# Kernel tuning notes

Measured on AMD Instinct MI355X. Metric: run time of the kernel, lower is better.

## Reference

```python
import jax, jax.numpy as jnp
import numpy as np

N = 50000        # nodes
E = 500000       # edges
NUM = 4          # sampled intermediate neighbors per edge (self.num)
F = 64           # in_feats == out_feats (transform=False)
D = 32           # dist_dim
NB = 64          # embedding rows = len(boundaries)+1


def setup_inputs() -> dict:
    key = jax.random.key(0)
    ks = jax.random.split(key, 10)
    feat = jax.random.normal(ks[0], (N, F), jnp.float32)
    loc = jax.random.uniform(ks[1], (N, 3), jnp.float32)          # 3D positions in unit cube
    boundaries = jnp.sort(jax.random.uniform(ks[2], (NB - 1,), jnp.float32, 0.0, 2.0))
    embed_table = jax.random.normal(ks[3], (NB, D), jnp.float32)
    G_w = jax.random.normal(ks[4], (F, D), jnp.float32) / np.sqrt(D)      # Linear(dist_dim->out, no bias)
    agg_w = jax.random.normal(ks[5], (F, 2 * F), jnp.float32) / np.sqrt(2 * F)  # Linear(2*out->out)
    agg_b = jnp.zeros((F,), jnp.float32)
    src = jax.random.randint(ks[6], (E,), 0, N, jnp.int32)
    dst = jax.random.randint(ks[7], (E,), 0, N, jnp.int32)
    inter_ids = jax.random.randint(ks[8], (E, NUM), 0, N, jnp.int32)
    return dict(feat=feat, loc=loc, boundaries=boundaries, embed_table=embed_table,
                G_w=G_w, agg_w=agg_w, agg_b=agg_b, src=src, dst=dst, inter_ids=inter_ids)


def reference(feat, loc, boundaries, embed_table, G_w, agg_w, agg_b, src, dst, inter_ids):
    n = feat.shape[0]
    ones = jnp.ones((src.shape[0],), feat.dtype)
    # symmetric-ish degree normalization: d0 = in_deg^-0.5, d2 = out_deg^-0.5
    in_deg = jax.ops.segment_sum(ones, dst, num_segments=n)
    out_deg = jax.ops.segment_sum(ones, src, num_segments=n)
    d0 = jnp.clip(in_deg, 1.0) ** -0.5   # [N]
    d2 = jnp.clip(out_deg, 1.0) ** -0.5  # [N]

    # dist1 = ||loc[dst] - loc[src]||_2, bucketize -> embed -> G
    dist1 = jnp.linalg.norm(loc[dst] - loc[src], axis=1)              # [E]
    de1 = embed_table[jnp.searchsorted(boundaries, dist1)] @ G_w.T    # [E, F]

    # intermediate sampled neighbors: dist to each sampled node from edge src
    pos_src = loc[src]                                                # [E, 3]
    inter_pos = loc[inter_ids]                                        # [E, NUM, 3]
    dist_ = jnp.linalg.norm(pos_src[:, None, :] - inter_pos, axis=-1) # [E, NUM]
    de_ = embed_table[jnp.searchsorted(boundaries, dist_)] @ G_w.T    # [E, NUM, F]
    inter_h = feat[inter_ids]                                         # [E, NUM, F]
    dist_embed_dot_h = (de_ * inter_h).mean(axis=1)                   # [E, F]

    # h = d0[dst] * d2[src] * agg_fc([de1 * h_src, dist_embed_dot_h])
    cat = jnp.concatenate([de1 * feat[src], dist_embed_dot_h], axis=1)  # [E, 2F]
    msg = (d0[dst] * d2[src])[:, None] * (cat @ agg_w.T + agg_b)        # [E, F]

    # update_all(copy_e('h'), sum) -> scatter-sum messages to dst
    ft = jax.ops.segment_sum(msg, dst, num_segments=n)                  # [N, F]
    return ft
```

## Files before the change

### kernel.cpp

```cpp
#include <hip/hip_runtime.h>
#include <math.h>

#define LUTN 1024
#define LUTSCALE 512.0f
#define NBINS 50048
#define CHSH 12


__global__ __launch_bounds__(256) void prep_kernel(
    const float* __restrict__ embed, const float* __restrict__ G_w,
    const float* __restrict__ boundaries, const float* __restrict__ feat,
    const float* __restrict__ loc,
    float* __restrict__ M, int* __restrict__ lut,
    unsigned short* __restrict__ featH, float4* __restrict__ loc4, int N) {

    const int gid = blockIdx.x * 256 + threadIdx.x;
    const int gsz = gridDim.x * 256;
    for (int i = gid; i < 4096; i += gsz) {
        int b = i >> 6, f = i & 63;
        float acc = 0.f;
        #pragma unroll
        for (int dd = 0; dd < 32; ++dd) acc += embed[b * 32 + dd] * G_w[f * 32 + dd];
        M[i] = acc;
    }
    for (int i = gid; i < LUTN; i += gsz) {
        float left = (float)i * (1.0f / LUTSCALE);
        int c = 0;
        for (int j = 0; j < 63; ++j) c += (boundaries[j] < left) ? 1 : 0;
        lut[i] = c;
    }
    const int nq = N * 16;
    for (int i = gid; i < nq; i += gsz) {
        float4 v = ((const float4*)feat)[i];
        unsigned ux = __float_as_uint(v.x), uy = __float_as_uint(v.y);
        unsigned uz = __float_as_uint(v.z), uw = __float_as_uint(v.w);
        ushort4 h;
        h.x = (unsigned short)((ux + 0x7FFFu + ((ux >> 16) & 1u)) >> 16);
        h.y = (unsigned short)((uy + 0x7FFFu + ((uy >> 16) & 1u)) >> 16);
        h.z = (unsigned short)((uz + 0x7FFFu + ((uz >> 16) & 1u)) >> 16);
        h.w = (unsigned short)((uw + 0x7FFFu + ((uw >> 16) & 1u)) >> 16);
        ((ushort4*)featH)[i] = h;
    }
    for (int i = gid; i < N; i += gsz)
        loc4[i] = make_float4(loc[3 * i], loc[3 * i + 1], loc[3 * i + 2], 0.f);
}


__global__ __launch_bounds__(512) void hist_kernel(
    const int* __restrict__ src, const int* __restrict__ dst,
    unsigned char* __restrict__ pcnt, unsigned char* __restrict__ psrc,
    unsigned char* __restrict__ rnk8, int E) {

    __shared__ unsigned int h[NBINS / 4];
    for (int i = threadIdx.x; i < NBINS / 4; i += 512) h[i] = 0u;
    __syncthreads();

    const int p    = blockIdx.x >> 1;
    const int role = blockIdx.x & 1;
    const int base = p << CHSH;
    const int lim  = min(E - base, 1 << CHSH);

    if (role == 0) {
        for (int t = threadIdx.x; t < lim; t += 512) {
            const int e = base + t;
            const int d = dst[e];
            const unsigned sh = (unsigned)(d & 3) * 8u;
            unsigned old = atomicAdd(&h[d >> 2], 1u << sh);
            rnk8[e] = (unsigned char)((old >> sh) & 0xFFu);
        }
        __syncthreads();
        unsigned int* gc = (unsigned int*)(pcnt + (size_t)p * NBINS);
        for (int i = threadIdx.x; i < NBINS / 4; i += 512) gc[i] = h[i];
    } else {
        for (int t = threadIdx.x; t < lim; t += 512) {
            const int s = src[base + t];
            atomicAdd(&h[s >> 2], 1u << ((unsigned)(s & 3) * 8u));
        }
        __syncthreads();
        unsigned int* gs = (unsigned int*)(psrc + (size_t)p * NBINS);
        for (int i = threadIdx.x; i < NBINS / 4; i += 512) gs[i] = h[i];
    }
}


__global__ __launch_bounds__(1024) void merge_scan_kernel(
    unsigned char* __restrict__ pcnt, const unsigned char* __restrict__ psrc,
    int* __restrict__ cnt, float* __restrict__ d2w,
    int* __restrict__ startv, int* __restrict__ part, int P, int N) {

    __shared__ int wsum[16];
    const int t = threadIdx.x, lane = t & 63, wv = t >> 6;
    const int d = blockIdx.x * 1024 + t;

    int sc = 0;
    if (d < N) {
        #pragma unroll 4
        for (int p = 0; p < P; ++p) {
            const size_t idx = (size_t)p * NBINS + d;
            const int c = pcnt[idx];
            pcnt[idx] = (unsigned char)sc;
            sc += c;
        }
        cnt[d] = sc;
        int ss = 0;
        #pragma unroll 4
        for (int p = 0; p < P; ++p) ss += psrc[(size_t)p * NBINS + d];
        d2w[d] = rsqrtf(fmaxf((float)ss, 1.0f));
    }

    const int v = sc;
    int x = v;
    #pragma unroll
    for (int off = 1; off < 64; off <<= 1) { int y = __shfl_up(x, off); if (lane >= off) x += y; }
    if (lane == 63) wsum[wv] = x;
    __syncthreads();
    if (t < 16) {
        int w = wsum[t], xx = w;
        #pragma unroll
        for (int off = 1; off < 16; off <<= 1) { int y = __shfl_up(xx, off); if (t >= off) xx += y; }
        wsum[t] = xx - w;
    }
    __syncthreads();
    int incl = x + wsum[wv];
    if (d < N) startv[d] = incl - v;
    if (t == 1023) part[blockIdx.x] = incl;
}

__device__ __forceinline__ void load_chunkoff(const int* __restrict__ part, int nb,
                                              int* __restrict__ co) {
    if (threadIdx.x < 64) {
        int v = (threadIdx.x < nb) ? part[threadIdx.x] : 0;
        int x = v;
        #pragma unroll
        for (int off = 1; off < 64; off <<= 1) {
            int y = __shfl_up(x, off);
            if ((threadIdx.x & 63) >= off) x += y;
        }
        co[threadIdx.x] = x - v;
    }
    __syncthreads();
}


__global__ __launch_bounds__(256) void edge_kernel(
    const float4* __restrict__ loc4, const float* __restrict__ boundaries,
    const int* __restrict__ lut,
    const int* __restrict__ src, const int* __restrict__ dst,
    const int* __restrict__ inter,
    const unsigned char* __restrict__ rnk8, const unsigned char* __restrict__ pcnt,
    const int* __restrict__ startv, const int* __restrict__ part,
    const float* __restrict__ d2w,
    int4* __restrict__ rec, int E, int nb) {

    __shared__ int lut_s[LUTN];
    __shared__ float bl[64];
    __shared__ int co[64];
    ((int4*)lut_s)[threadIdx.x] = ((const int4*)lut)[threadIdx.x];
    if (threadIdx.x < 64)
        bl[threadIdx.x] = (threadIdx.x < 63) ? boundaries[threadIdx.x] : 3.4e38f;
    load_chunkoff(part, nb, co);

    const int e = blockIdx.x * 256 + threadIdx.x;
    if (e >= E) return;

    const int s = src[e], d = dst[e];
    const int4 ii = ((const int4*)inter)[e];

    const float4 ps = loc4[s];
    float dist[5];
    {
        float4 pd = loc4[d];
        float dx = pd.x - ps.x, dy = pd.y - ps.y, dz = pd.z - ps.z;
        dist[0] = sqrtf(dx * dx + dy * dy + dz * dz);
    }
    const int id4[4] = {ii.x, ii.y, ii.z, ii.w};
    #pragma unroll
    for (int j = 0; j < 4; ++j) {
        float4 pt = loc4[id4[j]];
        float dx = pt.x - ps.x, dy = pt.y - ps.y, dz = pt.z - ps.z;
        dist[1 + j] = sqrtf(dx * dx + dy * dy + dz * dz);
    }
    unsigned pack = 0;
    #pragma unroll
    for (int q = 0; q < 5; ++q) {
        float dq = dist[q];
        int cell = (int)(dq * LUTSCALE);
        cell = (cell > LUTN - 1) ? (LUTN - 1) : cell;
        int b = lut_s[cell];
        while (b < 63 && bl[b] < dq) ++b;
        while (b > 0 && bl[b - 1] >= dq) --b;
        pack |= ((unsigned)b) << (6 * q);
    }

    const int p = e >> CHSH;
    const int cbase = pcnt[(size_t)p * NBINS + d];
    const int pos = startv[d] + co[d >> 10] + cbase + (int)rnk8[e];
    const float w = d2w[s];
    unsigned uw = __float_as_uint(w);
    unsigned wb = (uw + 0x7FFFu + ((uw >> 16) & 1u)) & 0xFFFF0000u;
    rec[pos] = make_int4(s | (ii.x << 16), ii.y | (ii.z << 16), ii.w | (int)wb, (int)pack);
}


__global__ __launch_bounds__(256) void node_kernel(
    const unsigned short* __restrict__ featH, const float* __restrict__ M,
    const int* __restrict__ cnt, const int* __restrict__ startv,
    const int* __restrict__ part, const int4* __restrict__ rec,
    float* __restrict__ cat, float* __restrict__ swb, int N, int nb) {

    __shared__ float Ms[4096];
    __shared__ int co[64];
    #pragma unroll
    for (int i = 0; i < 4; ++i)
        ((float4*)Ms)[threadIdx.x + 256 * i] = ((const float4*)M)[threadIdx.x + 256 * i];
    load_chunkoff(part, nb, co);

    const int lane = threadIdx.x & 63;
    const int wid  = threadIdx.x >> 6;
    const int gw   = blockIdx.x * 4 + wid;
    const int gstr = gridDim.x * 4;

    for (int d = gw; d < N; d += gstr) {
        const int deg  = __builtin_amdgcn_readfirstlane(cnt[d]);
        const int base = __builtin_amdgcn_readfirstlane(startv[d] + co[d >> 10]);
        const int4* rp = rec + base;

        float acc0 = 0.f, acc1 = 0.f, sw = 0.f;

        #pragma unroll 4
        for (int k = 0; k < deg; ++k) {
            const int4 r = rp[k];
            const int s  = r.x & 0xFFFF;
            const int i0 = ((unsigned)r.x) >> 16;
            const int i1 = r.y & 0xFFFF;
            const int i2 = ((unsigned)r.y) >> 16;
            const int i3 = r.z & 0xFFFF;
            const float w = __uint_as_float((unsigned)r.z & 0xFFFF0000u);
            const unsigned pk = (unsigned)r.w;

            const float fs = __uint_as_float(((unsigned)featH[(size_t)s  * 64 + lane]) << 16);
            const float f0 = __uint_as_float(((unsigned)featH[(size_t)i0 * 64 + lane]) << 16);
            const float f1 = __uint_as_float(((unsigned)featH[(size_t)i1 * 64 + lane]) << 16);
            const float f2 = __uint_as_float(((unsigned)featH[(size_t)i2 * 64 + lane]) << 16);
            const float f3 = __uint_as_float(((unsigned)featH[(size_t)i3 * 64 + lane]) << 16);
            const float m0 = Ms[(pk & 63u) * 64 + lane];
            const float m1 = Ms[((pk >> 6) & 63u) * 64 + lane];
            const float m2 = Ms[((pk >> 12) & 63u) * 64 + lane];
            const float m3 = Ms[((pk >> 18) & 63u) * 64 + lane];
            const float m4 = Ms[((pk >> 24) & 63u) * 64 + lane];

            acc0 = fmaf(m0 * fs, w, acc0);
            float t = m1 * f0 + m2 * f1 + m3 * f2 + m4 * f3;
            acc1 = fmaf(0.25f * t, w, acc1);
            sw += w;
        }

        cat[(size_t)d * 128 + lane]      = acc0;
        cat[(size_t)d * 128 + 64 + lane] = acc1;
        if (lane == 0) swb[d] = sw;
    }
}


__global__ __launch_bounds__(256) void epilogue_kernel(
    const float* __restrict__ cat, const float* __restrict__ agg_w,
    const float* __restrict__ agg_b, const float* __restrict__ swb,
    const int* __restrict__ cnt, float* __restrict__ out, int N) {

    const int lane = threadIdx.x & 63;
    const int wid  = threadIdx.x >> 6;

    float4 aw[32];
    const float4* awp = (const float4*)(agg_w + (size_t)lane * 128);
    #pragma unroll
    for (int i = 0; i < 32; ++i) aw[i] = awp[i];
    const float bias = agg_b[lane];

    const int gw = blockIdx.x * 4 + wid;
    const int stride = gridDim.x * 4;

    for (int d0i = gw; d0i < N; d0i += stride) {
        const int du = __builtin_amdgcn_readfirstlane(d0i);
        const float* cp = cat + (size_t)du * 128;
        float a0 = bias * swb[du], a1 = 0.f, a2 = 0.f, a3 = 0.f;
        #pragma unroll
        for (int k4 = 0; k4 < 32; k4 += 4) {
            float4 c0 = ((const float4*)cp)[k4];
            float4 c1 = ((const float4*)cp)[k4 + 1];
            float4 c2 = ((const float4*)cp)[k4 + 2];
            float4 c3 = ((const float4*)cp)[k4 + 3];
            a0 = fmaf(aw[k4].x, c0.x, a0); a0 = fmaf(aw[k4].y, c0.y, a0);
            a0 = fmaf(aw[k4].z, c0.z, a0); a0 = fmaf(aw[k4].w, c0.w, a0);
            a1 = fmaf(aw[k4+1].x, c1.x, a1); a1 = fmaf(aw[k4+1].y, c1.y, a1);
            a1 = fmaf(aw[k4+1].z, c1.z, a1); a1 = fmaf(aw[k4+1].w, c1.w, a1);
            a2 = fmaf(aw[k4+2].x, c2.x, a2); a2 = fmaf(aw[k4+2].y, c2.y, a2);
            a2 = fmaf(aw[k4+2].z, c2.z, a2); a2 = fmaf(aw[k4+2].w, c2.w, a2);
            a3 = fmaf(aw[k4+3].x, c3.x, a3); a3 = fmaf(aw[k4+3].y, c3.y, a3);
            a3 = fmaf(aw[k4+3].z, c3.z, a3); a3 = fmaf(aw[k4+3].w, c3.w, a3);
        }
        const float d0v = rsqrtf(fmaxf((float)cnt[du], 1.0f));
        out[(size_t)du * 64 + lane] = d0v * ((a0 + a1) + (a2 + a3));
    }
}


extern "C" void kernel_launch(void* const* d_in, const int* in_sizes, int n_in,
                              void* d_out, int out_size, void* d_ws, size_t ws_size,
                              hipStream_t stream) {
    const float* feat       = (const float*)d_in[0];
    const float* loc        = (const float*)d_in[1];
    const float* boundaries = (const float*)d_in[2];
    const float* embed      = (const float*)d_in[3];
    const float* G_w        = (const float*)d_in[4];
    const float* agg_w      = (const float*)d_in[5];
    const float* agg_b      = (const float*)d_in[6];
    const int*   src        = (const int*)d_in[7];
    const int*   dst        = (const int*)d_in[8];
    const int*   inter      = (const int*)d_in[9];

    const int N = in_sizes[0] / 64;
    const int E = in_sizes[7];

    const int P = (E + (1 << CHSH) - 1) >> CHSH;

    char* w = (char*)d_ws;
    auto take = [&](size_t bytes) { char* p = w; w += (bytes + 15) & ~(size_t)15; return p; };
    float*          M      = (float*)take(4096 * 4);
    int*            lut    = (int*)  take(LUTN * 4);
    int*            cnt    = (int*)  take((size_t)N * 4);
    int*            startv = (int*)  take((size_t)N * 4);
    int*            part   = (int*)  take(64 * 4);
    float*          d2w    = (float*)take((size_t)N * 4);
    int4*           rec    = (int4*) take((size_t)E * 16);
    unsigned char*  rnk8   = (unsigned char*)take((size_t)E);
    unsigned char*  pcnt   = (unsigned char*)take((size_t)P * NBINS);
    unsigned char*  psrc   = (unsigned char*)take((size_t)P * NBINS);
    float*          cat    = (float*)take((size_t)N * 128 * 4);
    float*          swb    = (float*)take((size_t)N * 4);
    unsigned short* featH  = (unsigned short*)take((size_t)N * 64 * 2);
    float4*         loc4   = (float4*)take((size_t)N * 16);
    float*          out    = (float*)d_out;

    const int eb = (E + 255) / 256;
    const int nb = (N + 1023) / 1024;

    prep_kernel<<<1024, 256, 0, stream>>>(embed, G_w, boundaries, feat, loc,
                                          M, lut, featH, loc4, N);
    hist_kernel<<<2 * P, 512, 0, stream>>>(src, dst, pcnt, psrc, rnk8, E);
    merge_scan_kernel<<<nb, 1024, 0, stream>>>(pcnt, psrc, cnt, d2w, startv, part, P, N);
    edge_kernel<<<eb, 256, 0, stream>>>(loc4, boundaries, lut, src, dst, inter,
                                        rnk8, pcnt, startv, part, d2w, rec, E, nb);
    node_kernel<<<2048, 256, 0, stream>>>(featH, M, cnt, startv, part, rec,
                                          cat, swb, N, nb);
    epilogue_kernel<<<768, 256, 0, stream>>>(cat, agg_w, agg_b, swb, cnt, out, N);
}
```

Before: 239.5 us.

## Fuse prep and histogram into one kernel; two edges per thread; one node per wave

Merges the prep kernel and the histogram kernel into a single launch whose first 2*P blocks do the histograms and whose remaining blocks do the prep work, removing one kernel launch and letting the two independent stages overlap. The edge kernel now handles two edges per thread with half as many blocks, which amortises the shared-memory LUT and boundary setup per block. The node kernel drops its grid-stride loop and launches one wave per destination node. Costs are a larger per-block shared allocation for the prep blocks, which can lower occupancy, and many more small node blocks to schedule.

Result: faster. 225.5 us (-5.8%).

```diff
diff --git a/kernel.cpp b/kernel.cpp
--- a/kernel.cpp
+++ b/kernel.cpp
@@ -7,15 +7,53 @@
 #define CHSH 12
 
 
-__global__ __launch_bounds__(256) void prep_kernel(
+__global__ __launch_bounds__(512) void front_kernel(
     const float* __restrict__ embed, const float* __restrict__ G_w,
     const float* __restrict__ boundaries, const float* __restrict__ feat,
     const float* __restrict__ loc,
+    const int* __restrict__ src, const int* __restrict__ dst,
     float* __restrict__ M, int* __restrict__ lut,
-    unsigned short* __restrict__ featH, float4* __restrict__ loc4, int N) {
-
-    const int gid = blockIdx.x * 256 + threadIdx.x;
-    const int gsz = gridDim.x * 256;
+    unsigned short* __restrict__ featH, float4* __restrict__ loc4,
+    unsigned char* __restrict__ pcnt, unsigned char* __restrict__ psrc,
+    unsigned char* __restrict__ rnk8,
+    int N, int E, int P, int PREPB) {
+
+    __shared__ unsigned int h[NBINS / 4];
+
+    if (blockIdx.x < 2 * P) {
+        for (int i = threadIdx.x; i < NBINS / 4; i += 512) h[i] = 0u;
+        __syncthreads();
+
+        const int p    = blockIdx.x >> 1;
+        const int role = blockIdx.x & 1;
+        const int base = p << CHSH;
+        const int lim  = min(E - base, 1 << CHSH);
+
+        if (role == 0) {
+            for (int t = threadIdx.x; t < lim; t += 512) {
+                const int e = base + t;
+                const int d = dst[e];
+                const unsigned sh = (unsigned)(d & 3) * 8u;
+                unsigned old = atomicAdd(&h[d >> 2], 1u << sh);
+                rnk8[e] = (unsigned char)((old >> sh) & 0xFFu);
+            }
+            __syncthreads();
+            unsigned int* gc = (unsigned int*)(pcnt + (size_t)p * NBINS);
+            for (int i = threadIdx.x; i < NBINS / 4; i += 512) gc[i] = h[i];
+        } else {
+            for (int t = threadIdx.x; t < lim; t += 512) {
+                const int s = src[base + t];
+                atomicAdd(&h[s >> 2], 1u << ((unsigned)(s & 3) * 8u));
+            }
+            __syncthreads();
+            unsigned int* gs = (unsigned int*)(psrc + (size_t)p * NBINS);
+            for (int i = threadIdx.x; i < NBINS / 4; i += 512) gs[i] = h[i];
+        }
+        return;
+    }
+
+    const int gid = (blockIdx.x - 2 * P) * 512 + threadIdx.x;
+    const int gsz = PREPB * 512;
     for (int i = gid; i < 4096; i += gsz) {
         int b = i >> 6, f = i & 63;
         float acc = 0.f;
@@ -34,52 +72,15 @@
         float4 v = ((const float4*)feat)[i];
         unsigned ux = __float_as_uint(v.x), uy = __float_as_uint(v.y);
         unsigned uz = __float_as_uint(v.z), uw = __float_as_uint(v.w);
-        ushort4 h;
-        h.x = (unsigned short)((ux + 0x7FFFu + ((ux >> 16) & 1u)) >> 16);
-        h.y = (unsigned short)((uy + 0x7FFFu + ((uy >> 16) & 1u)) >> 16);
-        h.z = (unsigned short)((uz + 0x7FFFu + ((uz >> 16) & 1u)) >> 16);
-        h.w = (unsigned short)((uw + 0x7FFFu + ((uw >> 16) & 1u)) >> 16);
-        ((ushort4*)featH)[i] = h;
+        ushort4 hh;
+        hh.x = (unsigned short)((ux + 0x7FFFu + ((ux >> 16) & 1u)) >> 16);
+        hh.y = (unsigned short)((uy + 0x7FFFu + ((uy >> 16) & 1u)) >> 16);
+        hh.z = (unsigned short)((uz + 0x7FFFu + ((uz >> 16) & 1u)) >> 16);
+        hh.w = (unsigned short)((uw + 0x7FFFu + ((uw >> 16) & 1u)) >> 16);
+        ((ushort4*)featH)[i] = hh;
     }
     for (int i = gid; i < N; i += gsz)
         loc4[i] = make_float4(loc[3 * i], loc[3 * i + 1], loc[3 * i + 2], 0.f);
-}
-
-
-__global__ __launch_bounds__(512) void hist_kernel(
-    const int* __restrict__ src, const int* __restrict__ dst,
-    unsigned char* __restrict__ pcnt, unsigned char* __restrict__ psrc,
-    unsigned char* __restrict__ rnk8, int E) {
-
-    __shared__ unsigned int h[NBINS / 4];
-    for (int i = threadIdx.x; i < NBINS / 4; i += 512) h[i] = 0u;
-    __syncthreads();
-
-    const int p    = blockIdx.x >> 1;
-    const int role = blockIdx.x & 1;
-    const int base = p << CHSH;
-    const int lim  = min(E - base, 1 << CHSH);
-
-    if (role == 0) {
-        for (int t = threadIdx.x; t < lim; t += 512) {
-            const int e = base + t;
-            const int d = dst[e];
-            const unsigned sh = (unsigned)(d & 3) * 8u;
-            unsigned old = atomicAdd(&h[d >> 2], 1u << sh);
-            rnk8[e] = (unsigned char)((old >> sh) & 0xFFu);
-        }
-        __syncthreads();
-        unsigned int* gc = (unsigned int*)(pcnt + (size_t)p * NBINS);
-        for (int i = threadIdx.x; i < NBINS / 4; i += 512) gc[i] = h[i];
-    } else {
-        for (int t = threadIdx.x; t < lim; t += 512) {
-            const int s = src[base + t];
-            atomicAdd(&h[s >> 2], 1u << ((unsigned)(s & 3) * 8u));
-        }
-        __syncthreads();
-        unsigned int* gs = (unsigned int*)(psrc + (size_t)p * NBINS);
-        for (int i = threadIdx.x; i < NBINS / 4; i += 512) gs[i] = h[i];
-    }
 }
 
 
@@ -160,45 +161,50 @@
         bl[threadIdx.x] = (threadIdx.x < 63) ? boundaries[threadIdx.x] : 3.4e38f;
     load_chunkoff(part, nb, co);
 
-    const int e = blockIdx.x * 256 + threadIdx.x;
-    if (e >= E) return;
-
-    const int s = src[e], d = dst[e];
-    const int4 ii = ((const int4*)inter)[e];
-
-    const float4 ps = loc4[s];
-    float dist[5];
-    {
-        float4 pd = loc4[d];
-        float dx = pd.x - ps.x, dy = pd.y - ps.y, dz = pd.z - ps.z;
-        dist[0] = sqrtf(dx * dx + dy * dy + dz * dz);
-    }
-    const int id4[4] = {ii.x, ii.y, ii.z, ii.w};
+    const int ebase = blockIdx.x * 512 + threadIdx.x;
+
     #pragma unroll
-    for (int j = 0; j < 4; ++j) {
-        float4 pt = loc4[id4[j]];
-        float dx = pt.x - ps.x, dy = pt.y - ps.y, dz = pt.z - ps.z;
-        dist[1 + j] = sqrtf(dx * dx + dy * dy + dz * dz);
-    }
-    unsigned pack = 0;
-    #pragma unroll
-    for (int q = 0; q < 5; ++q) {
-        float dq = dist[q];
-        int cell = (int)(dq * LUTSCALE);
-        cell = (cell > LUTN - 1) ? (LUTN - 1) : cell;
-        int b = lut_s[cell];
-        while (b < 63 && bl[b] < dq) ++b;
-        while (b > 0 && bl[b - 1] >= dq) --b;
-        pack |= ((unsigned)b) << (6 * q);
-    }
-
-    const int p = e >> CHSH;
-    const int cbase = pcnt[(size_t)p * NBINS + d];
-    const int pos = startv[d] + co[d >> 10] + cbase + (int)rnk8[e];
-    const float w = d2w[s];
-    unsigned uw = __float_as_uint(w);
-    unsigned wb = (uw + 0x7FFFu + ((uw >> 16) & 1u)) & 0xFFFF0000u;
-    rec[pos] = make_int4(s | (ii.x << 16), ii.y | (ii.z << 16), ii.w | (int)wb, (int)pack);
+    for (int u = 0; u < 2; ++u) {
+        const int e = ebase + u * 256;
+        if (e >= E) continue;
+
+        const int s = src[e], d = dst[e];
+        const int4 ii = ((const int4*)inter)[e];
+
+        const float4 ps = loc4[s];
+        float dist[5];
+        {
+            float4 pd = loc4[d];
+            float dx = pd.x - ps.x, dy = pd.y - ps.y, dz = pd.z - ps.z;
+            dist[0] = sqrtf(dx * dx + dy * dy + dz * dz);
+        }
+        const int id4[4] = {ii.x, ii.y, ii.z, ii.w};
+        #pragma unroll
+        for (int j = 0; j < 4; ++j) {
+            float4 pt = loc4[id4[j]];
+            float dx = pt.x - ps.x, dy = pt.y - ps.y, dz = pt.z - ps.z;
+            dist[1 + j] = sqrtf(dx * dx + dy * dy + dz * dz);
+        }
+        unsigned pack = 0;
+        #pragma unroll
+        for (int q = 0; q < 5; ++q) {
+            float dq = dist[q];
+            int cell = (int)(dq * LUTSCALE);
+            cell = (cell > LUTN - 1) ? (LUTN - 1) : cell;
+            int b = lut_s[cell];
+            while (b < 63 && bl[b] < dq) ++b;
+            while (b > 0 && bl[b - 1] >= dq) --b;
+            pack |= ((unsigned)b) << (6 * q);
+        }
+
+        const int p = e >> CHSH;
+        const int cbase = pcnt[(size_t)p * NBINS + d];
+        const int pos = startv[d] + co[d >> 10] + cbase + (int)rnk8[e];
+        const float w = d2w[s];
+        unsigned uw = __float_as_uint(w);
+        unsigned wb = (uw + 0x7FFFu + ((uw >> 16) & 1u)) & 0xFFFF0000u;
+        rec[pos] = make_int4(s | (ii.x << 16), ii.y | (ii.z << 16), ii.w | (int)wb, (int)pack);
+    }
 }
 
 
@@ -217,48 +223,46 @@
 
     const int lane = threadIdx.x & 63;
     const int wid  = threadIdx.x >> 6;
-    const int gw   = blockIdx.x * 4 + wid;
-    const int gstr = gridDim.x * 4;
-
-    for (int d = gw; d < N; d += gstr) {
-        const int deg  = __builtin_amdgcn_readfirstlane(cnt[d]);
-        const int base = __builtin_amdgcn_readfirstlane(startv[d] + co[d >> 10]);
-        const int4* rp = rec + base;
-
-        float acc0 = 0.f, acc1 = 0.f, sw = 0.f;
-
-        #pragma unroll 4
-        for (int k = 0; k < deg; ++k) {
-            const int4 r = rp[k];
-            const int s  = r.x & 0xFFFF;
-            const int i0 = ((unsigned)r.x) >> 16;
-            const int i1 = r.y & 0xFFFF;
-            const int i2 = ((unsigned)r.y) >> 16;
-            const int i3 = r.z & 0xFFFF;
-            const float w = __uint_as_float((unsigned)r.z & 0xFFFF0000u);
-            const unsigned pk = (unsigned)r.w;
-
-            const float fs = __uint_as_float(((unsigned)featH[(size_t)s  * 64 + lane]) << 16);
-            const float f0 = __uint_as_float(((unsigned)featH[(size_t)i0 * 64 + lane]) << 16);
-            const float f1 = __uint_as_float(((unsigned)featH[(size_t)i1 * 64 + lane]) << 16);
-            const float f2 = __uint_as_float(((unsigned)featH[(size_t)i2 * 64 + lane]) << 16);
-            const float f3 = __uint_as_float(((unsigned)featH[(size_t)i3 * 64 + lane]) << 16);
-            const float m0 = Ms[(pk & 63u) * 64 + lane];
-            const float m1 = Ms[((pk >> 6) & 63u) * 64 + lane];
-            const float m2 = Ms[((pk >> 12) & 63u) * 64 + lane];
-            const float m3 = Ms[((pk >> 18) & 63u) * 64 + lane];
-            const float m4 = Ms[((pk >> 24) & 63u) * 64 + lane];
-
-            acc0 = fmaf(m0 * fs, w, acc0);
-            float t = m1 * f0 + m2 * f1 + m3 * f2 + m4 * f3;
-            acc1 = fmaf(0.25f * t, w, acc1);
-            sw += w;
-        }
-
-        cat[(size_t)d * 128 + lane]      = acc0;
-        cat[(size_t)d * 128 + 64 + lane] = acc1;
-        if (lane == 0) swb[d] = sw;
-    }
+    const int d    = blockIdx.x * 4 + wid;
+    if (d >= N) return;
+
+    const int deg  = __builtin_amdgcn_readfirstlane(cnt[d]);
+    const int base = __builtin_amdgcn_readfirstlane(startv[d] + co[d >> 10]);
+    const int4* rp = rec + base;
+
+    float acc0 = 0.f, acc1 = 0.f, sw = 0.f;
+
+    #pragma unroll 4
+    for (int k = 0; k < deg; ++k) {
+        const int4 r = rp[k];
+        const int s  = r.x & 0xFFFF;
+        const int i0 = ((unsigned)r.x) >> 16;
+        const int i1 = r.y & 0xFFFF;
+        const int i2 = ((unsigned)r.y) >> 16;
+        const int i3 = r.z & 0xFFFF;
+        const float w = __uint_as_float((unsigned)r.z & 0xFFFF0000u);
+        const unsigned pk = (unsigned)r.w;
+
+        const float fs = __uint_as_float(((unsigned)featH[(size_t)s  * 64 + lane]) << 16);
+        const float f0 = __uint_as_float(((unsigned)featH[(size_t)i0 * 64 + lane]) << 16);
+        const float f1 = __uint_as_float(((unsigned)featH[(size_t)i1 * 64 + lane]) << 16);
+        const float f2 = __uint_as_float(((unsigned)featH[(size_t)i2 * 64 + lane]) << 16);
+        const float f3 = __uint_as_float(((unsigned)featH[(size_t)i3 * 64 + lane]) << 16);
+        const float m0 = Ms[(pk & 63u) * 64 + lane];
+        const float m1 = Ms[((pk >> 6) & 63u) * 64 + lane];
+        const float m2 = Ms[((pk >> 12) & 63u) * 64 + lane];
+        const float m3 = Ms[((pk >> 18) & 63u) * 64 + lane];
+        const float m4 = Ms[((pk >> 24) & 63u) * 64 + lane];
+
+        acc0 = fmaf(m0 * fs, w, acc0);
+        float t = m1 * f0 + m2 * f1 + m3 * f2 + m4 * f3;
+        acc1 = fmaf(0.25f * t, w, acc1);
+        sw += w;
+    }
+
+    cat[(size_t)d * 128 + lane]      = acc0;
+    cat[(size_t)d * 128 + 64 + lane] = acc1;
+    if (lane == 0) swb[d] = sw;
 }
 
 
@@ -341,16 +345,17 @@
     float4*         loc4   = (float4*)take((size_t)N * 16);
     float*          out    = (float*)d_out;
 
-    const int eb = (E + 255) / 256;
-    const int nb = (N + 1023) / 1024;
-
-    prep_kernel<<<1024, 256, 0, stream>>>(embed, G_w, boundaries, feat, loc,
-                                          M, lut, featH, loc4, N);
-    hist_kernel<<<2 * P, 512, 0, stream>>>(src, dst, pcnt, psrc, rnk8, E);
+    const int eb2 = (E + 511) / 512;
+    const int nb  = (N + 1023) / 1024;
+    const int PREPB = 256;
+
+    front_kernel<<<2 * P + PREPB, 512, 0, stream>>>(embed, G_w, boundaries, feat, loc,
+                                                    src, dst, M, lut, featH, loc4,
+                                                    pcnt, psrc, rnk8, N, E, P, PREPB);
     merge_scan_kernel<<<nb, 1024, 0, stream>>>(pcnt, psrc, cnt, d2w, startv, part, P, N);
-    edge_kernel<<<eb, 256, 0, stream>>>(loc4, boundaries, lut, src, dst, inter,
-                                        rnk8, pcnt, startv, part, d2w, rec, E, nb);
-    node_kernel<<<2048, 256, 0, stream>>>(featH, M, cnt, startv, part, rec,
-                                          cat, swb, N, nb);
+    edge_kernel<<<eb2, 256, 0, stream>>>(loc4, boundaries, lut, src, dst, inter,
+                                         rnk8, pcnt, startv, part, d2w, rec, E, nb);
+    node_kernel<<<(N + 3) / 4, 256, 0, stream>>>(featH, M, cnt, startv, part, rec,
+                                                 cat, swb, N, nb);
     epilogue_kernel<<<768, 256, 0, stream>>>(cat, agg_w, agg_b, swb, cnt, out, N);
 }
```
